# Kernel tuning notes

Measured on AMD Instinct MI355X. Metric: run time of the kernel, lower is better.

Reference implementation:

```python
import jax, jax.numpy as jnp
import numpy as np

B, L, D, DFF, MODES = 16, 1536, 512, 2048, 64
KERNELS = (3, 5, 7)


def setup_inputs() -> dict:
    key = jax.random.key(0)
    ks = jax.random.split(key, 12)
    scale = 1.0 / (D * D)
    f32 = jnp.float32
    return {
        "x": jax.random.normal(ks[0], (B, L, D), f32),
        "w_real": scale * jax.random.normal(ks[1], (D, D, MODES), f32),
        "w_imag": scale * jax.random.normal(ks[2], (D, D, MODES), f32),
        "conv1_w": jax.random.normal(ks[3], (DFF, D), f32) / np.sqrt(D).astype(np.float32),
        "conv2_w": jax.random.normal(ks[4], (D, DFF), f32) / np.sqrt(DFF).astype(np.float32),
        "d1_w1": jax.random.normal(ks[5], (D // 2, D), f32) / np.sqrt(D).astype(np.float32),
        "d1_b1": jnp.zeros((D // 2,), f32),
        "d1_w2": jax.random.normal(ks[6], (len(KERNELS), D // 2), f32) / np.sqrt(D // 2).astype(np.float32),
        "d1_b2": jnp.zeros((len(KERNELS),), f32),
        "d2_w1": jax.random.normal(ks[7], (D // 2, D), f32) / np.sqrt(D).astype(np.float32),
        "d2_b1": jnp.zeros((D // 2,), f32),
        "d2_w2": jax.random.normal(ks[8], (len(KERNELS), D // 2), f32) / np.sqrt(D // 2).astype(np.float32),
        "d2_b2": jnp.zeros((len(KERNELS),), f32),
    }


def _avg_pool1d(x, k):
    # torch AvgPool1d(kernel=k, stride=1, padding=k//2), count_include_pad=True:
    # zero-pad then divide by k everywhere. x: (B, L, D) -> (B, L, D) for odd k.
    pad = k // 2
    xp = jnp.pad(x, ((0, 0), (pad, pad), (0, 0)))
    cs = jnp.pad(jnp.cumsum(xp, axis=1), ((0, 0), (1, 0), (0, 0)))
    return (cs[:, k:, :] - cs[:, :-k, :]) / k


def _moe_decomp(x, w1, b1, w2, b2):
    # trends: (B, L, D, E)
    trends = jnp.stack([_avg_pool1d(x, k) for k in KERNELS], axis=-1)
    h = jax.nn.relu(jnp.einsum("bld,hd->blh", x, w1) + b1)
    logits = jnp.einsum("blh,eh->ble", h, w2) + b2
    gates = jax.nn.softmax(logits, axis=-1)[:, :, None, :]  # (B, L, 1, E)
    x_trend = jnp.sum(trends * gates, axis=-1)
    return x - x_trend  # seasonal component


def _fourier_block(x, w_real, w_imag):
    q_ft = jnp.fft.rfft(x, axis=1)  # (B, L//2+1, D) complex
    modes = min(MODES, q_ft.shape[1])
    weights = (w_real + 1j * w_imag).astype(jnp.complex64)  # (D, D, modes)
    # batched complex matmul over the kept modes (fuses the per-mode loop)
    out_m = jnp.einsum("bmd,dem->bme", q_ft[:, :modes, :], weights[:, :, :modes])
    out_ft = jnp.zeros((x.shape[0], x.shape[1] // 2 + 1, x.shape[2]), jnp.complex64)
    out_ft = out_ft.at[:, :modes, :].set(out_m)
    return jnp.fft.irfft(out_ft, n=x.shape[1], axis=1)


def reference(x, w_real, w_imag, conv1_w, conv2_w,
              d1_w1, d1_b1, d1_w2, d1_b2,
              d2_w1, d2_b1, d2_w2, d2_b2):
    # FEB-f + residual (dropout = identity in eval)
    x = x + _fourier_block(x, w_real, w_imag)
    x = _moe_decomp(x, d1_w1, d1_b1, d1_w2, d1_b2)
    # 1x1 conv FFN == per-token linear layers
    y = jax.nn.relu(jnp.einsum("bld,fd->blf", x, conv1_w))
    y = jnp.einsum("blf,df->bld", y, conv2_w)
    res = _moe_decomp(x + y, d2_w1, d2_b1, d2_w2, d2_b2)
    return res
```

## Files before the change

### kernel.cpp

```cpp
#include <hip/hip_runtime.h>

#define B_   16
#define L_   1536
#define D_   512
#define DFF_ 2048
#define NM   64
#define HID  256

typedef short short8  __attribute__((ext_vector_type(8)));
typedef short short4v __attribute__((ext_vector_type(4)));
typedef float f32x4   __attribute__((ext_vector_type(4)));

__device__ __forceinline__ float b2f(short s) {
  unsigned int u = ((unsigned int)(unsigned short)s) << 16;
  float f; __builtin_memcpy(&f, &u, 4); return f;
}
__device__ __forceinline__ short f2b(float f) {
  unsigned int u; __builtin_memcpy(&u, &f, 4);
  u += 0x7fffu + ((u >> 16) & 1u);
  return (short)(u >> 16);
}
__device__ __forceinline__ f32x4 zero4() {
  f32x4 v; v[0]=0.f; v[1]=0.f; v[2]=0.f; v[3]=0.f; return v;
}

#define MFMA(a,b,c) __builtin_amdgcn_mfma_f32_16x16x32_bf16((a),(b),(c),0,0,0)
#define SWZ(row, grp) (((row) << 6) + ((((grp) ^ ((row) & 7))) << 3))
#define GLDS16(gp, lp) __builtin_amdgcn_global_load_lds( \
    (const __attribute__((address_space(1))) void*)(gp), \
    (__attribute__((address_space(3))) void*)(lp), 16, 0, 0)

__global__ __launch_bounds__(256) void zero_out(float* __restrict__ o, int n) {
  int i = blockIdx.x * 256 + threadIdx.x;
  if (i < n) o[i] = 0.f;
}

__global__ __launch_bounds__(256) void prep_all(
    const float* __restrict__ conv1_w, const float* __restrict__ conv2_w,
    const float* __restrict__ d1_w1,  const float* __restrict__ d2_w1,
    short* __restrict__ c1, short* __restrict__ c2,
    short* __restrict__ dw1, short* __restrict__ dw2,
    short* __restrict__ tcs, short* __restrict__ basis)
{
  int blk = blockIdx.x;
  if (blk < 2304) {
    const float* s; short* d; int i;
    if (blk < 1024)      { s = conv1_w; d = c1;  i = blk * 256 + threadIdx.x; }
    else if (blk < 2048) { s = conv2_w; d = c2;  i = (blk - 1024) * 256 + threadIdx.x; }
    else if (blk < 2176) { s = d1_w1;   d = dw1; i = (blk - 2048) * 256 + threadIdx.x; }
    else                 { s = d2_w1;   d = dw2; i = (blk - 2176) * 256 + threadIdx.x; }
    f32x4 v = ((const f32x4*)s)[i];
    short4v o;
    #pragma unroll
    for (int j = 0; j < 4; ++j) o[j] = f2b(v[j]);
    ((short4v*)d)[i] = o;
    return;
  }
  if (blk < 3072) {
    int i = (blk - 2304) * 256 + threadIdx.x;
    int m = i / L_, l = i - m * L_;
    int mm = (m < 64) ? m : (m - 64);
    int r = (mm * l) % L_;
    float th = (float)r * (6.283185307179586f / (float)L_);
    float s, c; __sincosf(th, &s, &c);
    tcs[i] = f2b((m < 64) ? c : -s);
    return;
  }
  {
    int i = (blk - 3072) * 256 + threadIdx.x;
    int l = i >> 7, k = i & 127;
    int m = (k < 64) ? k : (k - 64);
    int r = (m * l) % L_;
    float th = (float)r * (6.283185307179586f / (float)L_);
    float s, c; __sincosf(th, &s, &c);
    float v = (k < 64) ? ((m == 0) ? 1.f : 2.f) * (1.f / (float)L_) * c
                       : (-2.f / (float)L_) * s;
    basis[i] = f2b(v);
  }
}

__global__ __launch_bounds__(256) void transpose_w(
    const float* __restrict__ wre, const float* __restrict__ wim,
    short* __restrict__ wtr, short* __restrict__ wti)
{
  __shared__ float tile[64][17];
  int dc = blockIdx.x, e = blockIdx.y, t = threadIdx.x;
  int zz = blockIdx.z;
  const float* w = (zz < 4) ? wre : wim;
  short* wt      = (zz < 4) ? wtr : wti;
  int mBase = (zz & 3) * 16;
  {
    int dl = t >> 2, mg = t & 3;
    f32x4 v = *(const f32x4*)(w + ((long)(dc * 64 + dl) * 512 + e) * 64 + mBase + mg * 4);
    tile[dl][mg*4+0] = v[0]; tile[dl][mg*4+1] = v[1];
    tile[dl][mg*4+2] = v[2]; tile[dl][mg*4+3] = v[3];
  }
  __syncthreads();
  if (t < 128) {
    int mr = t >> 3, dg = t & 7;
    short8 o;
    #pragma unroll
    for (int j = 0; j < 8; ++j) o[j] = f2b(tile[dg * 8 + j][mr]);
    *(short8*)(wt + ((long)(mBase + mr) * 512 + e) * 512 + dc * 64 + dg * 8) = o;
  }
}

__global__ __launch_bounds__(256) void transpose_x(const float* __restrict__ x,
                                                   short* __restrict__ xt) {
  __shared__ float tile[64][65];
  int dc = blockIdx.x, lc = blockIdx.y, b = blockIdx.z, t = threadIdx.x;
  const float* xb = x + (long)b * L_ * D_;
  #pragma unroll
  for (int i = 0; i < 4; ++i) {
    int idx = i * 256 + t; int ll = idx >> 4, dg = idx & 15;
    f32x4 v = *(const f32x4*)(xb + (long)(lc * 64 + ll) * D_ + dc * 64 + dg * 4);
    tile[ll][dg*4+0] = v[0]; tile[ll][dg*4+1] = v[1];
    tile[ll][dg*4+2] = v[2]; tile[ll][dg*4+3] = v[3];
  }
  __syncthreads();
  #pragma unroll
  for (int i = 0; i < 2; ++i) {
    int idx = i * 256 + t; int dl = idx >> 3, lg = idx & 7;
    short8 o;
    #pragma unroll
    for (int j = 0; j < 8; ++j) o[j] = f2b(tile[lg * 8 + j][dl]);
    *(short8*)(xt + ((long)b * D_ + dc * 64 + dl) * L_ + lc * 64 + lg * 8) = o;
  }
}

template<bool RELU, bool HASBIAS>
__global__ __launch_bounds__(256) void gemm64(
    const short* __restrict__ A, long ldA,
    const short* __restrict__ W, long ldW,
    const float* __restrict__ bias,
    short* __restrict__ outB, long csr, long csc, int K)
{
  __shared__ short lA[64 * 64];
  __shared__ short lW[64 * 64];
  const int t = threadIdx.x, lane = t & 63, wid = t >> 6;
  const int quad = lane >> 4, l15 = lane & 15;
  const int wm = (wid & 1) * 32, wn = (wid >> 1) * 32;
  const long row0 = (long)blockIdx.x * 64, col0 = (long)blockIdx.y * 64;
  const short* Ab = A + row0 * ldA;
  const short* Wb = W + col0 * ldW;

  int srcrow[2]; long srcoff[2];
  #pragma unroll
  for (int i = 0; i < 2; ++i) {
    int c = wid * 2 + i;
    int r = c * 8 + (lane >> 3);
    int g = (lane & 7) ^ (r & 7);
    srcrow[i] = r; srcoff[i] = g * 8;
  }

  f32x4 acc[2][2];
  #pragma unroll
  for (int i = 0; i < 2; ++i)
    #pragma unroll
    for (int j = 0; j < 2; ++j) acc[i][j] = zero4();

  for (int k0 = 0; k0 < K; k0 += 64) {
    __syncthreads();
    #pragma unroll
    for (int i = 0; i < 2; ++i) {
      int c = wid * 2 + i;
      GLDS16(Ab + (long)srcrow[i] * ldA + k0 + srcoff[i], lA + c * 512);
      GLDS16(Wb + (long)srcrow[i] * ldW + k0 + srcoff[i], lW + c * 512);
    }
    __syncthreads();
    #pragma unroll
    for (int ks = 0; ks < 2; ++ks) {
      int gq = ks * 4 + quad;
      short8 a0 = *(const short8*)&lA[SWZ(wm + l15, gq)];
      short8 a1 = *(const short8*)&lA[SWZ(wm + 16 + l15, gq)];
      short8 b0 = *(const short8*)&lW[SWZ(wn + l15, gq)];
      short8 b1 = *(const short8*)&lW[SWZ(wn + 16 + l15, gq)];
      acc[0][0] = MFMA(a0, b0, acc[0][0]);
      acc[0][1] = MFMA(a0, b1, acc[0][1]);
      acc[1][0] = MFMA(a1, b0, acc[1][0]);
      acc[1][1] = MFMA(a1, b1, acc[1][1]);
    }
  }
  #pragma unroll
  for (int ni = 0; ni < 2; ++ni) {
    long col = col0 + wn + ni * 16 + l15;
    float bvv = HASBIAS ? bias[col] : 0.f;
    #pragma unroll
    for (int mi = 0; mi < 2; ++mi) {
      #pragma unroll
      for (int r = 0; r < 4; ++r) {
        long row = row0 + wm + mi * 16 + quad * 4 + r;
        float v = acc[mi][ni][r];
        if (HASBIAS) v += bvv;
        if (RELU)    v = fmaxf(v, 0.f);
        outB[row * csr + col * csc] = f2b(v);
      }
    }
  }
}

template<bool RELU, bool HASBIAS, bool HASRES, bool RESB>
__global__ __launch_bounds__(256) void gemm128(
    const short* __restrict__ A, long ldA, long Az,
    const short* __restrict__ W, long ldW, long Wz,
    const float* __restrict__ bias,
    const void* __restrict__ res, long ldres, long resZ,
    short* __restrict__ outB, long ldC, long Cz, int K)
{
  __shared__ short lA[128 * 64];
  __shared__ short lW[128 * 64];
  const int t = threadIdx.x, lane = t & 63, wid = t >> 6;
  const int quad = lane >> 4, l15 = lane & 15;
  const int wm = (wid & 1) * 64, wn = (wid >> 1) * 64;
  const long row0 = (long)blockIdx.x * 128, col0 = (long)blockIdx.y * 128;
  const int z = blockIdx.z;
  const short* Ab = A + (long)z * Az + row0 * ldA;
  const short* Wb = W + (long)z * Wz + col0 * ldW;

  int srcrow[4]; long srcoff[4];
  #pragma unroll
  for (int i = 0; i < 4; ++i) {
    int c = wid * 4 + i;
    int r = c * 8 + (lane >> 3);
    int g = (lane & 7) ^ (r & 7);
    srcrow[i] = r; srcoff[i] = g * 8;
  }

  f32x4 acc[4][4];
  #pragma unroll
  for (int i = 0; i < 4; ++i)
    #pragma unroll
    for (int j = 0; j < 4; ++j) acc[i][j] = zero4();

  for (int k0 = 0; k0 < K; k0 += 64) {
    __syncthreads();
    #pragma unroll
    for (int i = 0; i < 4; ++i) {
      int c = wid * 4 + i;
      GLDS16(Ab + (long)srcrow[i] * ldA + k0 + srcoff[i], lA + c * 512);
      GLDS16(Wb + (long)srcrow[i] * ldW + k0 + srcoff[i], lW + c * 512);
    }
    __syncthreads();
    #pragma unroll
    for (int ks = 0; ks < 2; ++ks) {
      int gq = ks * 4 + quad;
      short8 av[4], bv[4];
      #pragma unroll
      for (int mi = 0; mi < 4; ++mi) av[mi] = *(const short8*)&lA[SWZ(wm + mi * 16 + l15, gq)];
      #pragma unroll
      for (int ni = 0; ni < 4; ++ni) bv[ni] = *(const short8*)&lW[SWZ(wn + ni * 16 + l15, gq)];
      #pragma unroll
      for (int mi = 0; mi < 4; ++mi)
        #pragma unroll
        for (int ni = 0; ni < 4; ++ni)
          acc[mi][ni] = MFMA(av[mi], bv[ni], acc[mi][ni]);
    }
  }
  #pragma unroll
  for (int ni = 0; ni < 4; ++ni) {
    long col = col0 + wn + ni * 16 + l15;
    float bvv = HASBIAS ? bias[col] : 0.f;
    #pragma unroll
    for (int mi = 0; mi < 4; ++mi) {
      #pragma unroll
      for (int r = 0; r < 4; ++r) {
        long row = row0 + wm + mi * 16 + quad * 4 + r;
        float v = acc[mi][ni][r];
        if (HASBIAS) v += bvv;
        if (RELU)    v = fmaxf(v, 0.f);
        if (HASRES) {
          long ro = (long)z * resZ + row * ldres + col;
          v += RESB ? b2f(((const short*)res)[ro]) : ((const float*)res)[ro];
        }
        outB[(long)z * Cz + row * ldC + col] = f2b(v);
      }
    }
  }
}

__global__ __launch_bounds__(256) void mode_gemm(
    const short* __restrict__ qr, const short* __restrict__ qi,
    const short* __restrict__ wr, const short* __restrict__ wi,
    short* __restrict__ outm)
{
  __shared__ short lqr[16 * 64], lqi[16 * 64], lwr[64 * 64], lwi[64 * 64];
  const int m = blockIdx.x, en = blockIdx.y;
  const int t = threadIdx.x, lane = t & 63, wid = t >> 6;
  const int quad = lane >> 4, l15 = lane & 15;
  const short* qrb = qr + (long)m * (B_ * D_);
  const short* qib = qi + (long)m * (B_ * D_);
  const short* wrb = wr + (long)m * (D_ * D_) + (long)en * 64 * D_;
  const short* wib = wi + (long)m * (D_ * D_) + (long)en * 64 * D_;
  f32x4 accr = zero4(), acci = zero4();
  for (int k0 = 0; k0 < D_; k0 += 64) {
    __syncthreads();
    {
      int idx = t & 127; int r = idx >> 3, cg = idx & 7;
      const short* src = (t < 128 ? qrb : qib) + r * D_ + k0 + cg * 8;
      short* dst = (t < 128) ? lqr : lqi;
      *(short8*)&dst[SWZ(r, cg)] = *(const short8*)src;
    }
    #pragma unroll
    for (int i = 0; i < 4; ++i) {
      int idx = i * 256 + t;
      int which = idx >> 9, idx2 = idx & 511;
      int r = idx2 >> 3, cg = idx2 & 7;
      const short* src = (which ? wib : wrb) + r * D_ + k0 + cg * 8;
      short* dst = which ? lwi : lwr;
      *(short8*)&dst[SWZ(r, cg)] = *(const short8*)src;
    }
    __syncthreads();
    #pragma unroll
    for (int ks = 0; ks < 2; ++ks) {
      int gq = ks * 4 + quad;
      short8 ar = *(const short8*)&lqr[SWZ(l15, gq)];
      short8 ai = *(const short8*)&lqi[SWZ(l15, gq)];
      short8 br = *(const short8*)&lwr[SWZ(wid * 16 + l15, gq)];
      short8 bi = *(const short8*)&lwi[SWZ(wid * 16 + l15, gq)];
      short8 nai;
      #pragma unroll
      for (int j = 0; j < 8; ++j) nai[j] = (short)(ai[j] ^ (short)0x8000);
      accr = MFMA(ar, br, accr);
      accr = MFMA(nai, bi, accr);
      acci = MFMA(ar, bi, acci);
      acci = MFMA(ai, br, acci);
    }
  }
  #pragma unroll
  for (int r = 0; r < 4; ++r) {
    int bb = quad * 4 + r;
    long e = (long)en * 64 + wid * 16 + l15;
    long base = ((long)bb * D_ + e) * 128 + m;
    outm[base]      = f2b(accr[r]);
    outm[base + 64] = f2b(acci[r]);
  }
}

template<bool OUTF, bool WRITEB>
__global__ __launch_bounds__(512) void combine_kernel(
    const short* __restrict__ xin, const short* __restrict__ h,
    const float* __restrict__ w2, const float* __restrict__ b2,
    float* __restrict__ outf, short* __restrict__ outb)
{
  __shared__ float lG[64][4];
  int lc = blockIdx.x, b = blockIdx.y, t = threadIdx.x;
  int wid = t >> 6, lane = t & 63;
  int l0 = lc * 64;
  #pragma unroll
  for (int pi = 0; pi < 8; ++pi) {
    int pos = wid * 8 + pi;
    long row = (long)b * L_ + l0 + pos;
    short4v hh = *(const short4v*)(h + row * HID + lane * 4);
    float hv[4];
    #pragma unroll
    for (int j = 0; j < 4; ++j) hv[j] = b2f(hh[j]);
    float lg[3];
    #pragma unroll
    for (int e = 0; e < 3; ++e) {
      const float* wrow = w2 + e * HID + lane * 4;
      float p = hv[0] * wrow[0] + hv[1] * wrow[1] + hv[2] * wrow[2] + hv[3] * wrow[3];
      #pragma unroll
      for (int off = 32; off >= 1; off >>= 1) p += __shfl_xor(p, off);
      lg[e] = p + b2[e];
    }
    float mx = fmaxf(lg[0], fmaxf(lg[1], lg[2]));
    float e0 = __expf(lg[0] - mx), e1 = __expf(lg[1] - mx), e2 = __expf(lg[2] - mx);
    float inv = 1.f / (e0 + e1 + e2);
    float gv = (lane == 0) ? e0 * inv : (lane == 1) ? e1 * inv : e2 * inv;
    if (lane < 3) lG[pos][lane] = gv;
  }
  __syncthreads();

  int d = t;
  const short* xb = xin + (long)b * L_ * D_ + d;
  float win[7];
  #pragma unroll
  for (int j = 0; j < 6; ++j) {
    int l = l0 - 3 + j;
    win[j] = (l >= 0 && l < L_) ? b2f(xb[(long)l * D_]) : 0.f;
  }
  for (int i = 0; i < 64; ++i) {
    int lcn = l0 + i;
    int lr = lcn + 3;
    win[6] = (lr < L_) ? b2f(xb[(long)lr * D_]) : 0.f;
    float s3 = win[2] + win[3] + win[4];
    float s5 = s3 + win[1] + win[5];
    float s7 = s5 + win[0] + win[6];
    float trend = lG[i][0] * s3 * (1.f / 3.f) + lG[i][1] * s5 * (1.f / 5.f)
                + lG[i][2] * s7 * (1.f / 7.f);
    float v = win[3] - trend;
    long o = ((long)b * L_ + lcn) * D_ + d;
    if (OUTF)   outf[o] = v;
    if (WRITEB) outb[o] = f2b(v);
    #pragma unroll
    for (int j = 0; j < 6; ++j) win[j] = win[j + 1];
  }
}

extern "C" void kernel_launch(void* const* d_in, const int* in_sizes, int n_in,
                              void* d_out, int out_size, void* d_ws, size_t ws_size,
                              hipStream_t stream) {
  const float* x       = (const float*)d_in[0];
  const float* w_real  = (const float*)d_in[1];
  const float* w_imag  = (const float*)d_in[2];
  const float* conv1_w = (const float*)d_in[3];
  const float* conv2_w = (const float*)d_in[4];
  const float* d1_w1   = (const float*)d_in[5];
  const float* d1_b1   = (const float*)d_in[6];
  const float* d1_w2   = (const float*)d_in[7];
  const float* d1_b2   = (const float*)d_in[8];
  const float* d2_w1   = (const float*)d_in[9];
  const float* d2_b1   = (const float*)d_in[10];
  const float* d2_w2   = (const float*)d_in[11];
  const float* d2_b2   = (const float*)d_in[12];
  float* OUT = (float*)d_out;

  const size_t REQ_BIG = 144703488, REQ_SMALL = 98566144;
  if (ws_size < REQ_SMALL) {
    zero_out<<<(out_size + 255) / 256, 256, 0, stream>>>(OUT, out_size);
    return;
  }
  const bool big = (ws_size >= REQ_BIG);

  char* ws = (char*)d_ws;
  short* C1WB  = (short*)(ws + 0);
  short* C2WB  = (short*)(ws + 2097152);
  short* D1W1B = (short*)(ws + 4194304);
  short* D2W1B = (short*)(ws + 4456448);
  short* TCS   = (short*)(ws + 4718592);
  short* BASIS = (short*)(ws + 5111808);
  short* XT    = (short*)(ws + 6291456);
  short* Y1    = XT;
  short* QRI   = (short*)(ws + 31457280);
  short* OUTM  = (short*)(ws + 33554432);
  short* WTR   = (short*)(ws + 35651584);
  short* X1B   = WTR;
  short* WTI   = (short*)(ws + 69206016);
  short* X2B   = (short*)(ws + (big ? 106954752 : 60817408));
  short* H     = (short*)(ws + (big ? 132120576 : 85983232));

  prep_all<<<3840, 256, 0, stream>>>(conv1_w, conv2_w, d1_w1, d2_w1,
                                     C1WB, C2WB, D1W1B, D2W1B, TCS, BASIS);
  transpose_w<<<dim3(8, 512, 8), 256, 0, stream>>>(w_real, w_imag, WTR, WTI);
  transpose_x<<<dim3(8, 24, 16), 256, 0, stream>>>(x, XT);

  gemm64<false, false><<<dim3(128, 2), 256, 0, stream>>>(
      XT, L_, TCS, L_, nullptr, QRI, 1, (long)B_ * D_, L_);

  mode_gemm<<<dim3(64, 8), 256, 0, stream>>>(QRI, QRI + 64 * B_ * D_, WTR, WTI, OUTM);

  gemm128<false, false, true, false><<<dim3(12, 4, 16), 256, 0, stream>>>(
      BASIS, 128, 0, OUTM, 128, (long)D_ * 128, nullptr,
      x, D_, (long)L_ * D_, X1B, D_, (long)L_ * D_, 128);

  gemm64<true, true><<<dim3(384, 4), 256, 0, stream>>>(
      X1B, D_, D1W1B, D_, d1_b1, H, HID, 1, D_);
  combine_kernel<false, true><<<dim3(24, 16), 512, 0, stream>>>(
      X1B, H, d1_w2, d1_b2, nullptr, X2B);

  {
    const int nchunk = big ? 1 : 2;
    const long rows = big ? 24576 : 12288;
    for (int rc = 0; rc < nchunk; ++rc) {
      short* Ain = X2B + (long)rc * rows * D_;
      gemm128<true, false, false, false><<<dim3(rows / 128, 16, 1), 256, 0, stream>>>(
          Ain, D_, 0, C1WB, D_, 0, nullptr, nullptr, 0, 0, Y1, DFF_, 0, D_);
      gemm128<false, false, true, true><<<dim3(rows / 128, 4, 1), 256, 0, stream>>>(
          Y1, DFF_, 0, C2WB, DFF_, 0, nullptr, Ain, D_, 0, Ain, D_, 0, DFF_);
    }
  }

  gemm64<true, true><<<dim3(384, 4), 256, 0, stream>>>(
      X2B, D_, D2W1B, D_, d2_b1, H, HID, 1, D_);
  combine_kernel<true, false><<<dim3(24, 16), 512, 0, stream>>>(
      X2B, H, d2_w2, d2_b2, OUT, nullptr);
}
```

Measured before the change: 628.8 us.

## Double-buffer LDS tiles in gemm64 and gemm128 to overlap loads with MFMA

Both GEMM kernels now keep two LDS buffers per operand and prefetch the next two K-tiles with direct global-to-LDS loads. Explicit vmcnt waits and raw barriers replace the two __syncthreads per iteration, so the next tile's load can run while MFMAs consume the current one. This hides global memory latency but doubles LDS use per block, which can lower occupancy (gemm128 grows to 64KB), and correctness now relies on the hand-counted vmcnt values.

```diff
diff --git a/kernel.cpp b/kernel.cpp
--- a/kernel.cpp
+++ b/kernel.cpp
@@ -135,8 +135,8 @@
     const float* __restrict__ bias,
     short* __restrict__ outB, long csr, long csc, int K)
 {
-  __shared__ short lA[64 * 64];
-  __shared__ short lW[64 * 64];
+  __shared__ short lA[2][64 * 64];
+  __shared__ short lW[2][64 * 64];
   const int t = threadIdx.x, lane = t & 63, wid = t >> 6;
   const int quad = lane >> 4, l15 = lane & 15;
   const int wm = (wid & 1) * 32, wn = (wid >> 1) * 32;
@@ -159,28 +159,54 @@
     #pragma unroll
     for (int j = 0; j < 2; ++j) acc[i][j] = zero4();
 
-  for (int k0 = 0; k0 < K; k0 += 64) {
-    __syncthreads();
+  const int nk = K >> 6;
+  #pragma unroll
+  for (int i = 0; i < 2; ++i) {
+    int c = wid * 2 + i;
+    GLDS16(Ab + (long)srcrow[i] * ldA + srcoff[i], lA[0] + c * 512);
+    GLDS16(Wb + (long)srcrow[i] * ldW + srcoff[i], lW[0] + c * 512);
+  }
+  if (nk > 1) {
     #pragma unroll
     for (int i = 0; i < 2; ++i) {
       int c = wid * 2 + i;
-      GLDS16(Ab + (long)srcrow[i] * ldA + k0 + srcoff[i], lA + c * 512);
-      GLDS16(Wb + (long)srcrow[i] * ldW + k0 + srcoff[i], lW + c * 512);
-    }
-    __syncthreads();
+      GLDS16(Ab + (long)srcrow[i] * ldA + 64 + srcoff[i], lA[1] + c * 512);
+      GLDS16(Wb + (long)srcrow[i] * ldW + 64 + srcoff[i], lW[1] + c * 512);
+    }
+  }
+
+  for (int it = 0; it < nk; ++it) {
+    if (it + 1 < nk) asm volatile("s_waitcnt vmcnt(4)" ::: "memory");
+    else             asm volatile("s_waitcnt vmcnt(0)" ::: "memory");
+    __builtin_amdgcn_s_barrier();
+    const int cur = it & 1;
+    const short* bufA = lA[cur];
+    const short* bufW = lW[cur];
     #pragma unroll
     for (int ks = 0; ks < 2; ++ks) {
       int gq = ks * 4 + quad;
-      short8 a0 = *(const short8*)&lA[SWZ(wm + l15, gq)];
-      short8 a1 = *(const short8*)&lA[SWZ(wm + 16 + l15, gq)];
-      short8 b0 = *(const short8*)&lW[SWZ(wn + l15, gq)];
-      short8 b1 = *(const short8*)&lW[SWZ(wn + 16 + l15, gq)];
+      short8 a0 = *(const short8*)&bufA[SWZ(wm + l15, gq)];
+      short8 a1 = *(const short8*)&bufA[SWZ(wm + 16 + l15, gq)];
+      short8 b0 = *(const short8*)&bufW[SWZ(wn + l15, gq)];
+      short8 b1 = *(const short8*)&bufW[SWZ(wn + 16 + l15, gq)];
       acc[0][0] = MFMA(a0, b0, acc[0][0]);
       acc[0][1] = MFMA(a0, b1, acc[0][1]);
       acc[1][0] = MFMA(a1, b0, acc[1][0]);
       acc[1][1] = MFMA(a1, b1, acc[1][1]);
     }
-  }
+    asm volatile("s_waitcnt lgkmcnt(0)" ::: "memory");
+    __builtin_amdgcn_s_barrier();
+    const long kn = (long)(it + 2) * 64;
+    if (kn < K) {
+      #pragma unroll
+      for (int i = 0; i < 2; ++i) {
+        int c = wid * 2 + i;
+        GLDS16(Ab + (long)srcrow[i] * ldA + kn + srcoff[i], lA[cur] + c * 512);
+        GLDS16(Wb + (long)srcrow[i] * ldW + kn + srcoff[i], lW[cur] + c * 512);
+      }
+    }
+  }
+
   #pragma unroll
   for (int ni = 0; ni < 2; ++ni) {
     long col = col0 + wn + ni * 16 + l15;
@@ -207,8 +233,8 @@
     const void* __restrict__ res, long ldres, long resZ,
     short* __restrict__ outB, long ldC, long Cz, int K)
 {
-  __shared__ short lA[128 * 64];
-  __shared__ short lW[128 * 64];
+  __shared__ short lA[2][128 * 64];
+  __shared__ short lW[2][128 * 64];
   const int t = threadIdx.x, lane = t & 63, wid = t >> 6;
   const int quad = lane >> 4, l15 = lane & 15;
   const int wm = (wid & 1) * 64, wn = (wid >> 1) * 64;
@@ -232,30 +258,56 @@
     #pragma unroll
     for (int j = 0; j < 4; ++j) acc[i][j] = zero4();
 
-  for (int k0 = 0; k0 < K; k0 += 64) {
-    __syncthreads();
+  const int nk = K >> 6;
+  #pragma unroll
+  for (int i = 0; i < 4; ++i) {
+    int c = wid * 4 + i;
+    GLDS16(Ab + (long)srcrow[i] * ldA + srcoff[i], lA[0] + c * 512);
+    GLDS16(Wb + (long)srcrow[i] * ldW + srcoff[i], lW[0] + c * 512);
+  }
+  if (nk > 1) {
     #pragma unroll
     for (int i = 0; i < 4; ++i) {
       int c = wid * 4 + i;
-      GLDS16(Ab + (long)srcrow[i] * ldA + k0 + srcoff[i], lA + c * 512);
-      GLDS16(Wb + (long)srcrow[i] * ldW + k0 + srcoff[i], lW + c * 512);
-    }
-    __syncthreads();
+      GLDS16(Ab + (long)srcrow[i] * ldA + 64 + srcoff[i], lA[1] + c * 512);
+      GLDS16(Wb + (long)srcrow[i] * ldW + 64 + srcoff[i], lW[1] + c * 512);
+    }
+  }
+
+  for (int it = 0; it < nk; ++it) {
+    if (it + 1 < nk) asm volatile("s_waitcnt vmcnt(8)" ::: "memory");
+    else             asm volatile("s_waitcnt vmcnt(0)" ::: "memory");
+    __builtin_amdgcn_s_barrier();
+    const int cur = it & 1;
+    const short* bufA = lA[cur];
+    const short* bufW = lW[cur];
     #pragma unroll
     for (int ks = 0; ks < 2; ++ks) {
       int gq = ks * 4 + quad;
       short8 av[4], bv[4];
       #pragma unroll
-      for (int mi = 0; mi < 4; ++mi) av[mi] = *(const short8*)&lA[SWZ(wm + mi * 16 + l15, gq)];
-      #pragma unroll
-      for (int ni = 0; ni < 4; ++ni) bv[ni] = *(const short8*)&lW[SWZ(wn + ni * 16 + l15, gq)];
+      for (int mi = 0; mi < 4; ++mi) av[mi] = *(const short8*)&bufA[SWZ(wm + mi * 16 + l15, gq)];
+      #pragma unroll
+      for (int ni = 0; ni < 4; ++ni) bv[ni] = *(const short8*)&bufW[SWZ(wn + ni * 16 + l15, gq)];
       #pragma unroll
       for (int mi = 0; mi < 4; ++mi)
         #pragma unroll
         for (int ni = 0; ni < 4; ++ni)
           acc[mi][ni] = MFMA(av[mi], bv[ni], acc[mi][ni]);
     }
-  }
+    asm volatile("s_waitcnt lgkmcnt(0)" ::: "memory");
+    __builtin_amdgcn_s_barrier();
+    const long kn = (long)(it + 2) * 64;
+    if (kn < K) {
+      #pragma unroll
+      for (int i = 0; i < 4; ++i) {
+        int c = wid * 4 + i;
+        GLDS16(Ab + (long)srcrow[i] * ldA + kn + srcoff[i], lA[cur] + c * 512);
+        GLDS16(Wb + (long)srcrow[i] * ldW + kn + srcoff[i], lW[cur] + c * 512);
+      }
+    }
+  }
+
   #pragma unroll
   for (int ni = 0; ni < 4; ++ni) {
     long col = col0 + wn + ni * 16 + l15;
```

New measurement: 631.0 us. About the same (+0.3%).
